# Kernel optimization log

Measured on AMD Instinct MI355X. Metric: run time of the kernel, lower is better.

The kernel has to match this reference:

```python
import jax, jax.numpy as jnp
import numpy as np

B, N, DIM = 4, 8192, 512
HEADS, DIM_HEAD = 8, 64
INNER = HEADS * DIM_HEAD
SCALE = DIM_HEAD ** -0.5


def setup_inputs() -> dict:
    key = jax.random.key(0)
    ks = jax.random.split(key, 8)
    return {
        "x": jax.random.normal(ks[0], (B, N, DIM), jnp.float32),
        "mask": jnp.zeros((B, N), jnp.bool_),
        "W_qkv": jax.random.normal(ks[1], (3 * INNER, DIM), jnp.float32) * 0.02,
        "w_q_logits": jax.random.normal(ks[2], (DIM_HEAD,), jnp.float32) * 0.02,
        "w_k_logits": jax.random.normal(ks[3], (DIM_HEAD,), jnp.float32) * 0.02,
        "W_r": jax.random.normal(ks[4], (DIM_HEAD, DIM_HEAD), jnp.float32) * 0.02,
        "b_r": jnp.zeros((DIM_HEAD,), jnp.float32),
        "W_out": jax.random.normal(ks[5], (DIM, INNER), jnp.float32) * 0.02,
        "b_out": jnp.zeros((DIM,), jnp.float32),
    }


def reference(x, mask, W_qkv, w_q_logits, w_k_logits, W_r, b_r, W_out, b_out):
    b, n, _ = x.shape
    neg_inf = jnp.float32(-jnp.inf)
    qkv = x @ W_qkv.T                              # (b, n, 3*inner)
    q, k, v = jnp.split(qkv, 3, axis=-1)           # each (b, n, inner)
    # faithful to torch: contiguous().view(b, heads, n, dim_head) == plain reshape
    q = q.reshape(b, HEADS, n, DIM_HEAD)
    k = k.reshape(b, HEADS, n, DIM_HEAD)
    v = v.reshape(b, HEADS, n, DIM_HEAD)
    m = mask[:, None, :]                           # (b, 1, n)

    # query pooling -> global query vector
    q_logits = jnp.einsum('bhnd,d->bhn', q, w_q_logits) * SCALE
    q_attn = jax.nn.softmax(jnp.where(m, neg_inf, q_logits), axis=-1)
    global_q = jnp.einsum('bhn,bhnd->bhd', q_attn, q)   # (b, h, d)

    # gate keys with global query, pool -> global key vector
    kg = k * global_q[:, :, None, :]
    k_logits = jnp.einsum('bhnd,d->bhn', kg, w_k_logits) * SCALE
    k_attn = jax.nn.softmax(jnp.where(m, neg_inf, k_logits), axis=-1)
    global_k = jnp.einsum('bhn,bhnd->bhd', k_attn, k)   # pools original k (k_agg)

    # gate values with global key, project, residual with q
    vg = v * global_k[:, :, None, :]
    r = vg @ W_r.T + b_r + q                            # (b, h, n, d)
    r = r.reshape(b, n, INNER)
    return r @ W_out.T + b_out
```

## Files before the change

kernel.cpp:

```cpp
#include <hip/hip_runtime.h>
#include <cstdint>

#define NB    4
#define NSEQ  8192
#define NDIM  512
#define NHEAD 8
#define DH    64
#define NTOK  (NB * NSEQ)
#define QKV_W 1536
#define SCALE 0.125f

typedef unsigned short u16;
typedef __attribute__((ext_vector_type(8))) unsigned short u16x8;
typedef __attribute__((ext_vector_type(4))) unsigned short u16x4;
typedef __attribute__((ext_vector_type(8))) short s16x8;
typedef __attribute__((ext_vector_type(4))) float f32x4;

__device__ __forceinline__ float bf2f(u16 u) {
  return __uint_as_float(((unsigned int)u) << 16);
}
__device__ __forceinline__ u16 f2bf(float f) {
  unsigned int x = __float_as_uint(f);
  x += 0x7fffu + ((x >> 16) & 1u);
  return (u16)(x >> 16);
}
__device__ __forceinline__ void gload_lds16(const void* g, void* l) {
  __builtin_amdgcn_global_load_lds(
      (const __attribute__((address_space(1))) unsigned int*)g,
      (__attribute__((address_space(3))) unsigned int*)l, 16, 0, 0);
}

__global__ __launch_bounds__(256) void cvt_bf16(
    const float* __restrict__ s0, u16* __restrict__ d0, int n0,
    const float* __restrict__ s1, u16* __restrict__ d1, int n1,
    const float* __restrict__ s2, u16* __restrict__ d2, int n2) {
  int gid = blockIdx.x * 256 + threadIdx.x;
  int stride = gridDim.x * 256;
  int t0 = n0 >> 2, t1 = n1 >> 2, t2 = n2 >> 2;
  for (int i = gid; i < t0; i += stride) {
    f32x4 v = ((const f32x4*)s0)[i];
    u16x4 o; o[0]=f2bf(v[0]); o[1]=f2bf(v[1]); o[2]=f2bf(v[2]); o[3]=f2bf(v[3]);
    ((u16x4*)d0)[i] = o;
  }
  for (int i = gid; i < t1; i += stride) {
    f32x4 v = ((const f32x4*)s1)[i];
    u16x4 o; o[0]=f2bf(v[0]); o[1]=f2bf(v[1]); o[2]=f2bf(v[2]); o[3]=f2bf(v[3]);
    ((u16x4*)d1)[i] = o;
  }
  for (int i = gid; i < t2; i += stride) {
    f32x4 v = ((const f32x4*)s2)[i];
    u16x4 o; o[0]=f2bf(v[0]); o[1]=f2bf(v[1]); o[2]=f2bf(v[2]); o[3]=f2bf(v[3]);
    ((u16x4*)d2)[i] = o;
  }
}

__global__ __launch_bounds__(512, 2) void gemm256(
    const u16* __restrict__ A, const u16* __restrict__ B,
    int K, int tiles_n,
    u16* __restrict__ Cbf, float* __restrict__ Cf,
    const float* __restrict__ bias) {
  __shared__ u16 lds[65536];
  const int KT = K >> 6;

  const int nwg = gridDim.x, bid = blockIdx.x;
  const int cpx = nwg >> 3;
  const int swz = (bid & 7) * cpx + (bid >> 3);
  const int tm = swz / tiles_n, tn = swz - tm * tiles_n;

  const int tid = threadIdx.x, lane = tid & 63, wid = tid >> 6;
  const int wm = wid >> 2, wn = wid & 3;
  const int rA = lane & 15, kq = lane >> 4, swl = lane & 7;

  const u16* Ab = A + (size_t)tm * 256 * K;
  const u16* Bb = B + (size_t)tn * 256 * K;

  auto STAGE = [&](int isB, int d, int h, int kt) {
    const u16* src = isB ? Bb : Ab;
    const int base = (isB ? 32768 : 0) + (d * 2 + h) * 8192;
#pragma unroll
    for (int r = 0; r < 2; ++r) {
      const int slot = r * 512 + tid;
      const int row = slot >> 3, ch = slot & 7;
      gload_lds16(src + (size_t)(h * 128 + row) * K + kt * 64 +
                      ((ch ^ (row & 7)) << 3),
                  &lds[base + slot * 8]);
    }
  };

  f32x4 acc[8][4] = {};

  STAGE(0, 0, 0, 0); STAGE(0, 0, 1, 0);
  STAGE(1, 0, 0, 0); STAGE(1, 0, 1, 0);
  {
    const int k1 = (KT > 1) ? 1 : 0;
    STAGE(1, 1, 0, k1); STAGE(1, 1, 1, k1);
  }
  asm volatile("s_waitcnt vmcnt(4)" ::: "memory");
  __builtin_amdgcn_s_barrier();

#define LDA(m, kk) (*(const s16x8*)&lds[Abase + ((m) * 16 + rA) * 64 + \
                                        ((((kk) * 4 + kq) ^ swl) << 3)])
#define LDB(n, kk) (*(const s16x8*)&lds[Bbase + (brow + (n) * 16 + rA) * 64 + \
                                        ((((kk) * 4 + kq) ^ swl) << 3)])
#define MFMA_(a, b, c) __builtin_amdgcn_mfma_f32_16x16x32_bf16(a, b, c, 0, 0, 0)

#define PHASE(M0, M1, BREAD, STG, TAIL)                                  \
  {                                                                      \
    s16x8 a00 = LDA(M0, 0), a01 = LDA(M0, 1);                            \
    s16x8 a10 = LDA(M1, 0), a11 = LDA(M1, 1);                            \
    BREAD                                                                \
    STG                                                                  \
    __builtin_amdgcn_s_barrier();                                        \
    asm volatile("s_waitcnt lgkmcnt(0)" ::: "memory");                   \
    __builtin_amdgcn_s_setprio(1);                                       \
    acc[M0][0] = MFMA_(a00, b00, acc[M0][0]);                            \
    acc[M0][0] = MFMA_(a01, b01, acc[M0][0]);                            \
    acc[M0][1] = MFMA_(a00, b10, acc[M0][1]);                            \
    acc[M0][1] = MFMA_(a01, b11, acc[M0][1]);                            \
    acc[M0][2] = MFMA_(a00, b20, acc[M0][2]);                            \
    acc[M0][2] = MFMA_(a01, b21, acc[M0][2]);                            \
    acc[M0][3] = MFMA_(a00, b30, acc[M0][3]);                            \
    acc[M0][3] = MFMA_(a01, b31, acc[M0][3]);                            \
    acc[M1][0] = MFMA_(a10, b00, acc[M1][0]);                            \
    acc[M1][0] = MFMA_(a11, b01, acc[M1][0]);                            \
    acc[M1][1] = MFMA_(a10, b10, acc[M1][1]);                            \
    acc[M1][1] = MFMA_(a11, b11, acc[M1][1]);                            \
    acc[M1][2] = MFMA_(a10, b20, acc[M1][2]);                            \
    acc[M1][2] = MFMA_(a11, b21, acc[M1][2]);                            \
    acc[M1][3] = MFMA_(a10, b30, acc[M1][3]);                            \
    acc[M1][3] = MFMA_(a11, b31, acc[M1][3]);                            \
    __builtin_amdgcn_s_setprio(0);                                       \
    TAIL                                                                 \
    __builtin_amdgcn_s_barrier();                                        \
  }

  for (int t = 0; t < KT; ++t) {
    const int d = t & 1;
    const int kA = (t + 1 < KT) ? t + 1 : KT - 1;
    const int kB = (t + 2 < KT) ? t + 2 : KT - 1;
    const int Abase = (d * 2 + wm) * 8192;
    const int Bbase = 32768 + (d * 2 + (wn >> 1)) * 8192;
    const int brow = (wn & 1) * 64;

    s16x8 b00, b01, b10, b11, b20, b21, b30, b31;

    PHASE(0, 1,
          { b00 = LDB(0, 0); b01 = LDB(0, 1); b10 = LDB(1, 0); b11 = LDB(1, 1);
            b20 = LDB(2, 0); b21 = LDB(2, 1); b30 = LDB(3, 0); b31 = LDB(3, 1); },
          STAGE(0, d ^ 1, 0, kA);, )
    PHASE(2, 3, , STAGE(0, d ^ 1, 1, kA);, )
    PHASE(4, 5, , STAGE(1, d, 0, kB);, )
    PHASE(6, 7, , STAGE(1, d, 1, kB);,
          asm volatile("s_waitcnt vmcnt(4)" ::: "memory");)
  }

  asm volatile("s_waitcnt vmcnt(0)" ::: "memory");

  const int crow = kq * 4;
  const int ccol = rA;
  const size_t row_base = (size_t)tm * 256 + wm * 128;
  const int col_base = tn * 256 + wn * 64;
  const int N = tiles_n << 8;
  if (Cbf) {
#pragma unroll
    for (int m = 0; m < 8; ++m)
#pragma unroll
      for (int n = 0; n < 4; ++n)
#pragma unroll
        for (int j = 0; j < 4; ++j)
          Cbf[(row_base + m * 16 + crow + j) * N + col_base + n * 16 + ccol] =
              f2bf(acc[m][n][j]);
  } else {
#pragma unroll
    for (int m = 0; m < 8; ++m)
#pragma unroll
      for (int n = 0; n < 4; ++n) {
        int col = col_base + n * 16 + ccol;
        float bv = bias[col];
#pragma unroll
        for (int j = 0; j < 4; ++j)
          Cf[(row_base + m * 16 + crow + j) * N + col] = acc[m][n][j] + bv;
      }
  }
#undef LDA
#undef LDB
#undef MFMA_
#undef PHASE
}

__global__ __launch_bounds__(256) void pool_stage(
    const u16* __restrict__ qkv, int chan_off,
    const float* __restrict__ wvec, float scale,
    float* __restrict__ partS, float* __restrict__ partG) {
  __shared__ float redG[4][64];
  __shared__ float redS[4];
  const int bid = blockIdx.x;
  const int bh = bid >> 3, chunk = bid & 7;
  const int b = bh >> 3, h = bh & 7;
  const int tid = threadIdx.x, lane = tid & 63, w = tid >> 6;
  const int j = lane & 7;

  float wreg[8];
#pragma unroll
  for (int i = 0; i < 8; ++i) wreg[i] = wvec[j * 8 + i];

  float accS = 0.f;
  float accG[8] = {};
  const size_t tok0 = (size_t)b * NSEQ + (size_t)h * 1024 + chunk * 128;

  for (int it = 0; it < 32; ++it) {
    const u16* row = qkv + (tok0 + it * 4 + w) * QKV_W + chan_off;
    u16x8 q8 = *(const u16x8*)(row + lane * 8);
    float qf[8];
#pragma unroll
    for (int i = 0; i < 8; ++i) qf[i] = bf2f(q8[i]);
    float dot = 0.f;
#pragma unroll
    for (int i = 0; i < 8; ++i) dot += qf[i] * wreg[i];
    dot += __shfl_xor(dot, 1);
    dot += __shfl_xor(dot, 2);
    dot += __shfl_xor(dot, 4);
    float e = __expf(dot * scale);
    accS += (j == 0) ? e : 0.f;
#pragma unroll
    for (int i = 0; i < 8; ++i) accG[i] += e * qf[i];
  }
#pragma unroll
  for (int m = 8; m <= 32; m <<= 1) {
    accS += __shfl_xor(accS, m);
#pragma unroll
    for (int i = 0; i < 8; ++i) accG[i] += __shfl_xor(accG[i], m);
  }
  if (lane < 8) {
#pragma unroll
    for (int i = 0; i < 8; ++i) redG[w][lane * 8 + i] = accG[i];
    if (lane == 0) redS[w] = accS;
  }
  __syncthreads();
  if (tid < 64) {
    float G = redG[0][tid] + redG[1][tid] + redG[2][tid] + redG[3][tid];
    partG[(size_t)bid * 64 + tid] = G;
    if (tid == 0) partS[bid] = redS[0] + redS[1] + redS[2] + redS[3];
  }
}

__global__ __launch_bounds__(64) void finalize_pool(
    const float* __restrict__ partS, const float* __restrict__ partG,
    const float* __restrict__ mulvec, float scale,
    float* __restrict__ outv) {
  int bh = blockIdx.x, d = threadIdx.x;
  float S = 0.f, G = 0.f;
#pragma unroll
  for (int c = 0; c < 8; ++c) {
    S += partS[bh * 8 + c];
    G += partG[(bh * 8 + c) * 64 + d];
  }
  float g = G / S;
  if (mulvec) g *= mulvec[d] * scale;
  outv[bh * 64 + d] = g;
}

__global__ __launch_bounds__(256) void r_stage(
    const u16* __restrict__ qkv, const float* __restrict__ gk,
    const float* __restrict__ W_r, const float* __restrict__ b_r,
    u16* __restrict__ rout) {
  __shared__ float M2T[64 * 64];
  const int t0 = blockIdx.x * 32;
  const int bh = (t0 >> 13) * 8 + ((t0 & 8191) >> 10);
  const int tid = threadIdx.x;
  for (int idx = tid; idx < 4096; idx += 256) {
    int e = idx >> 6, d = idx & 63;
    M2T[idx] = W_r[d * 64 + e] * gk[bh * 64 + e];
  }
  __syncthreads();

  const int t = t0 + (tid >> 3), g = tid & 7;
  const u16* vrow = qkv + (size_t)t * QKV_W + 1024 + g * 64;
  const u16* qrow = qkv + (size_t)t * QKV_W + g * 64;

  f32x4 acc[16] = {};
  for (int ec = 0; ec < 8; ++ec) {
    u16x8 v8 = *(const u16x8*)(vrow + ec * 8);
#pragma unroll
    for (int eo = 0; eo < 8; ++eo) {
      float ve = bf2f(v8[eo]);
      const f32x4* m2row = (const f32x4*)(M2T + (ec * 8 + eo) * 64);
#pragma unroll
      for (int c4 = 0; c4 < 16; ++c4) acc[c4] += ve * m2row[c4];
    }
  }
#pragma unroll
  for (int i = 0; i < 8; ++i) {
    u16x8 q8 = *(const u16x8*)(qrow + i * 8);
    u16x8 o;
#pragma unroll
    for (int ii = 0; ii < 8; ++ii) {
      int d = i * 8 + ii;
      float val = bf2f(q8[ii]) + b_r[d] + acc[d >> 2][d & 3];
      o[ii] = f2bf(val);
    }
    *(u16x8*)(rout + (size_t)t * NDIM + g * 64 + i * 8) = o;
  }
}

extern "C" void kernel_launch(void* const* d_in, const int* in_sizes, int n_in,
                              void* d_out, int out_size, void* d_ws,
                              size_t ws_size, hipStream_t stream) {
  const float* x    = (const float*)d_in[0];
  const float* Wqkv = (const float*)d_in[2];
  const float* wq   = (const float*)d_in[3];
  const float* wk   = (const float*)d_in[4];
  const float* Wr   = (const float*)d_in[5];
  const float* br   = (const float*)d_in[6];
  const float* Wout = (const float*)d_in[7];
  const float* bout = (const float*)d_in[8];
  float* out = (float*)d_out;

  char* w = (char*)d_ws;
  auto carve = [&](size_t bytes) {
    char* p = w;
    w += (bytes + 255) & ~(size_t)255;
    return p;
  };
  u16* x_bf    = (u16*)carve((size_t)NTOK * NDIM * 2);
  u16* qkv_bf  = (u16*)carve((size_t)NTOK * QKV_W * 2);
  u16* Wqkv_bf = (u16*)carve((size_t)QKV_W * NDIM * 2);
  u16* Wout_bf = (u16*)carve((size_t)NDIM * NDIM * 2);
  float* partS  = (float*)carve(256 * 4);
  float* partG  = (float*)carve(256 * 64 * 4);
  float* wk_eff = (float*)carve(32 * 64 * 4);
  float* gk     = (float*)carve(32 * 64 * 4);
  u16* r_bf    = x_bf;

  cvt_bf16<<<2048, 256, 0, stream>>>(x, x_bf, NTOK * NDIM,
                                     Wqkv, Wqkv_bf, QKV_W * NDIM,
                                     Wout, Wout_bf, NDIM * NDIM);
  gemm256<<<128 * 6, 512, 0, stream>>>(x_bf, Wqkv_bf, NDIM, 6,
                                       qkv_bf, nullptr, nullptr);
  pool_stage<<<256, 256, 0, stream>>>(qkv_bf, 0, wq, SCALE, partS, partG);
  finalize_pool<<<32, 64, 0, stream>>>(partS, partG, wk, SCALE, wk_eff);
  pool_stage<<<256, 256, 0, stream>>>(qkv_bf, 512, wk_eff, 1.0f, partS, partG);
  finalize_pool<<<32, 64, 0, stream>>>(partS, partG, nullptr, 1.0f, gk);
  r_stage<<<NTOK / 32, 256, 0, stream>>>(qkv_bf, gk, Wr, br, r_bf);
  gemm256<<<128 * 2, 512, 0, stream>>>(r_bf, Wout_bf, NDIM, 2,
                                       nullptr, out, bout);
}
```

Measured before the change: 318.5 us.

## Compute gated value projection with bf16 MFMA instead of scalar FMA

The r-stage scalar fp32 FMA loop over a shared-memory M2T matrix is replaced by a small prep kernel and an MFMA kernel. The prep kernel folds the global-key gate into W_r per (batch, head) and stores it as bf16. The MFMA kernel keeps those weights in registers and runs 16x16x32 bf16 MFMAs over rows of V. This moves the per-token 64x64 matmul off the vector ALUs and removes the LDS staging, at the cost of one extra launch and rounding the gated weights to bf16.

```diff
diff --git a/kernel.cpp b/kernel.cpp
--- a/kernel.cpp
+++ b/kernel.cpp
@@ -260,47 +260,72 @@
   outv[bh * 64 + d] = g;
 }
 
-__global__ __launch_bounds__(256) void r_stage(
-    const u16* __restrict__ qkv, const float* __restrict__ gk,
-    const float* __restrict__ W_r, const float* __restrict__ b_r,
-    u16* __restrict__ rout) {
-  __shared__ float M2T[64 * 64];
-  const int t0 = blockIdx.x * 32;
-  const int bh = (t0 >> 13) * 8 + ((t0 & 8191) >> 10);
-  const int tid = threadIdx.x;
-  for (int idx = tid; idx < 4096; idx += 256) {
-    int e = idx >> 6, d = idx & 63;
-    M2T[idx] = W_r[d * 64 + e] * gk[bh * 64 + e];
-  }
-  __syncthreads();
-
-  const int t = t0 + (tid >> 3), g = tid & 7;
-  const u16* vrow = qkv + (size_t)t * QKV_W + 1024 + g * 64;
-  const u16* qrow = qkv + (size_t)t * QKV_W + g * 64;
-
-  f32x4 acc[16] = {};
-  for (int ec = 0; ec < 8; ++ec) {
-    u16x8 v8 = *(const u16x8*)(vrow + ec * 8);
-#pragma unroll
-    for (int eo = 0; eo < 8; ++eo) {
-      float ve = bf2f(v8[eo]);
-      const f32x4* m2row = (const f32x4*)(M2T + (ec * 8 + eo) * 64);
-#pragma unroll
-      for (int c4 = 0; c4 < 16; ++c4) acc[c4] += ve * m2row[c4];
+__global__ __launch_bounds__(256) void weff_prep(
+    const float* __restrict__ Wr, const float* __restrict__ gk,
+    u16* __restrict__ weff) {
+  const int bh = blockIdx.x, tid = threadIdx.x;
+  for (int i = tid; i < 4096; i += 256) {
+    int e = i & 63;
+    weff[bh * 4096 + i] = f2bf(Wr[i] * gk[bh * 64 + e]);
+  }
+}
+
+__global__ __launch_bounds__(256) void r_mfma(
+    const u16* __restrict__ qkv, const u16* __restrict__ weff,
+    const float* __restrict__ b_r, u16* __restrict__ rout) {
+  const int tid = threadIdx.x, lane = tid & 63, wv = tid >> 6;
+  const size_t rho0 = (size_t)blockIdx.x * 256 + wv * 64;
+  const int bh = (int)(rho0 >> 13);
+  const int rA = lane & 15, kq = lane >> 4;
+
+#define MFMA_(a, b, c) __builtin_amdgcn_mfma_f32_16x16x32_bf16(a, b, c, 0, 0, 0)
+
+  s16x8 af[4][2];
+  const u16* wb = weff + bh * 4096;
+#pragma unroll
+  for (int fm = 0; fm < 4; ++fm)
+#pragma unroll
+    for (int kk = 0; kk < 2; ++kk)
+      af[fm][kk] = *(const s16x8*)(wb + (fm * 16 + rA) * 64 + kk * 32 + kq * 8);
+
+  f32x4 br4[4];
+#pragma unroll
+  for (int fm = 0; fm < 4; ++fm)
+    br4[fm] = *(const f32x4*)(b_r + fm * 16 + kq * 4);
+
+  f32x4 acc[4][4] = {};
+#pragma unroll
+  for (int fn = 0; fn < 4; ++fn) {
+    const size_t rho = rho0 + fn * 16 + rA;
+    const u16* vr = qkv + (rho >> 3) * QKV_W + 1024 + (rho & 7) * 64;
+    s16x8 b0 = *(const s16x8*)(vr + kq * 8);
+    s16x8 b1 = *(const s16x8*)(vr + 32 + kq * 8);
+#pragma unroll
+    for (int fm = 0; fm < 4; ++fm) {
+      acc[fm][fn] = MFMA_(af[fm][0], b0, acc[fm][fn]);
+      acc[fm][fn] = MFMA_(af[fm][1], b1, acc[fm][fn]);
     }
   }
-#pragma unroll
-  for (int i = 0; i < 8; ++i) {
-    u16x8 q8 = *(const u16x8*)(qrow + i * 8);
-    u16x8 o;
-#pragma unroll
-    for (int ii = 0; ii < 8; ++ii) {
-      int d = i * 8 + ii;
-      float val = bf2f(q8[ii]) + b_r[d] + acc[d >> 2][d & 3];
-      o[ii] = f2bf(val);
+
+#pragma unroll
+  for (int fn = 0; fn < 4; ++fn) {
+    const size_t rho = rho0 + fn * 16 + rA;
+    const size_t t = rho >> 3;
+    const int g = (int)(rho & 7);
+    const u16* qr = qkv + t * QKV_W + g * 64;
+    u16* orow = rout + t * NDIM + g * 64;
+#pragma unroll
+    for (int fm = 0; fm < 4; ++fm) {
+      const int d0 = fm * 16 + kq * 4;
+      u16x4 q4 = *(const u16x4*)(qr + d0);
+      u16x4 o;
+#pragma unroll
+      for (int j = 0; j < 4; ++j)
+        o[j] = f2bf(acc[fm][fn][j] + br4[fm][j] + bf2f(q4[j]));
+      *(u16x4*)(orow + d0) = o;
     }
-    *(u16x8*)(rout + (size_t)t * NDIM + g * 64 + i * 8) = o;
-  }
+  }
+#undef MFMA_
 }
 
 extern "C" void kernel_launch(void* const* d_in, const int* in_sizes, int n_in,
@@ -330,6 +355,7 @@
   float* partG  = (float*)carve(256 * 64 * 4);
   float* wk_eff = (float*)carve(32 * 64 * 4);
   float* gk     = (float*)carve(32 * 64 * 4);
+  u16* weff    = (u16*)carve(32 * 64 * 64 * 2);
   u16* r_bf    = x_bf;
 
   cvt_bf16<<<2048, 256, 0, stream>>>(x, x_bf, NTOK * NDIM,
@@ -341,7 +367,8 @@
   finalize_pool<<<32, 64, 0, stream>>>(partS, partG, wk, SCALE, wk_eff);
   pool_stage<<<256, 256, 0, stream>>>(qkv_bf, 512, wk_eff, 1.0f, partS, partG);
   finalize_pool<<<32, 64, 0, stream>>>(partS, partG, nullptr, 1.0f, gk);
-  r_stage<<<NTOK / 32, 256, 0, stream>>>(qkv_bf, gk, Wr, br, r_bf);
+  weff_prep<<<32, 256, 0, stream>>>(Wr, gk, weff);
+  r_mfma<<<NTOK * 8 / 256, 256, 0, stream>>>(qkv_bf, weff, br, r_bf);
   gemm256<<<128 * 2, 512, 0, stream>>>(r_bf, Wout_bf, NDIM, 2,
                                        nullptr, out, bout);
 }
```

Result: faster. 274.7 us (-13.8%).

## Fold W_r and global-key gating into per-head output weights, drop r_stage

Applied to the files above, without the earlier changes.

Precomputes P = W_out·blockdiag(W_r) and a combined bias vector, then builds per-(batch,head-group) concatenated weights that fold the global-key gating into P. The final GEMM reads v and q directly from the qkv buffer with K=1024, which removes the r_stage kernel and its intermediate write and read. The pooling stages are also split into 4x more blocks for parallelism. The cost is doubling K in the output GEMM, 32 per-batch weight copies, and an extra prep computation over the weight matrices.

```diff
diff --git a/kernel.cpp b/kernel.cpp
--- a/kernel.cpp
+++ b/kernel.cpp
@@ -30,27 +30,41 @@
       (__attribute__((address_space(3))) unsigned int*)l, 16, 0, 0);
 }
 
-__global__ __launch_bounds__(256) void cvt_bf16(
-    const float* __restrict__ s0, u16* __restrict__ d0, int n0,
-    const float* __restrict__ s1, u16* __restrict__ d1, int n1,
-    const float* __restrict__ s2, u16* __restrict__ d2, int n2) {
+__global__ __launch_bounds__(256) void prep(
+    const float* __restrict__ x, u16* __restrict__ x_bf,
+    const float* __restrict__ Wqkv, u16* __restrict__ Wqkv_bf,
+    const float* __restrict__ Wout, const float* __restrict__ Wr,
+    float* __restrict__ P,
+    const float* __restrict__ br, const float* __restrict__ bout,
+    float* __restrict__ cvec) {
   int gid = blockIdx.x * 256 + threadIdx.x;
   int stride = gridDim.x * 256;
-  int t0 = n0 >> 2, t1 = n1 >> 2, t2 = n2 >> 2;
+  int t0 = (NTOK * NDIM) >> 2;
   for (int i = gid; i < t0; i += stride) {
-    f32x4 v = ((const f32x4*)s0)[i];
+    f32x4 v = ((const f32x4*)x)[i];
     u16x4 o; o[0]=f2bf(v[0]); o[1]=f2bf(v[1]); o[2]=f2bf(v[2]); o[3]=f2bf(v[3]);
-    ((u16x4*)d0)[i] = o;
-  }
+    ((u16x4*)x_bf)[i] = o;
+  }
+  int t1 = (QKV_W * NDIM) >> 2;
   for (int i = gid; i < t1; i += stride) {
-    f32x4 v = ((const f32x4*)s1)[i];
+    f32x4 v = ((const f32x4*)Wqkv)[i];
     u16x4 o; o[0]=f2bf(v[0]); o[1]=f2bf(v[1]); o[2]=f2bf(v[2]); o[3]=f2bf(v[3]);
-    ((u16x4*)d1)[i] = o;
-  }
-  for (int i = gid; i < t2; i += stride) {
-    f32x4 v = ((const f32x4*)s2)[i];
-    u16x4 o; o[0]=f2bf(v[0]); o[1]=f2bf(v[1]); o[2]=f2bf(v[2]); o[3]=f2bf(v[3]);
-    ((u16x4*)d2)[i] = o;
+    ((u16x4*)Wqkv_bf)[i] = o;
+  }
+  for (int i = gid; i < 512 * 512; i += stride) {
+    int o = i >> 9, ii = i & 511;
+    int g = ii >> 6, e = ii & 63;
+    const float* wo = Wout + o * 512 + g * 64;
+    float s = 0.f;
+#pragma unroll 8
+    for (int d = 0; d < 64; ++d) s += wo[d] * Wr[d * 64 + e];
+    P[i] = s;
+  }
+  for (int o = gid; o < 512; o += stride) {
+    float s = bout[o];
+    const float* wo = Wout + o * 512;
+    for (int i2 = 0; i2 < 512; ++i2) s += wo[i2] * br[i2 & 63];
+    cvec[o] = s;
   }
 }
 
@@ -188,6 +202,133 @@
 #undef PHASE
 }
 
+__global__ __launch_bounds__(512, 2) void gemm_out(
+    const u16* __restrict__ qkv, const u16* __restrict__ Wcat,
+    const float* __restrict__ cvec, float* __restrict__ out) {
+  __shared__ u16 lds[65536];
+  const int KT = 16;
+
+  const int nwg = gridDim.x, bid = blockIdx.x;
+  const int cpx = nwg >> 3;
+  const int swz = (bid & 7) * cpx + (bid >> 3);
+  const int tm = swz >> 1, tn = swz & 1;
+
+  const int tid = threadIdx.x, lane = tid & 63, wid = tid >> 6;
+  const int wm = wid >> 2, wn = wid & 3;
+  const int rA = lane & 15, kq = lane >> 4, swl = lane & 7;
+
+  const u16* Bb = Wcat + ((size_t)(tm >> 2) * 512 + tn * 256) * 1024;
+
+  auto STAGEA = [&](int d, int h, int kt) {
+    const int base = (d * 2 + h) * 8192;
+    const int col0 = (kt < 8) ? (1024 + kt * 64) : ((kt - 8) * 64);
+#pragma unroll
+    for (int r = 0; r < 2; ++r) {
+      const int slot = r * 512 + tid;
+      const int row = slot >> 3, ch = slot & 7;
+      gload_lds16(qkv + (size_t)(tm * 256 + h * 128 + row) * QKV_W + col0 +
+                      ((ch ^ (row & 7)) << 3),
+                  &lds[base + slot * 8]);
+    }
+  };
+  auto STAGEB = [&](int d, int h, int kt) {
+    const int base = 32768 + (d * 2 + h) * 8192;
+#pragma unroll
+    for (int r = 0; r < 2; ++r) {
+      const int slot = r * 512 + tid;
+      const int row = slot >> 3, ch = slot & 7;
+      gload_lds16(Bb + (size_t)(h * 128 + row) * 1024 + kt * 64 +
+                      ((ch ^ (row & 7)) << 3),
+                  &lds[base + slot * 8]);
+    }
+  };
+
+  f32x4 acc[8][4] = {};
+
+  STAGEA(0, 0, 0); STAGEA(0, 1, 0);
+  STAGEB(0, 0, 0); STAGEB(0, 1, 0);
+  STAGEB(1, 0, 1); STAGEB(1, 1, 1);
+  asm volatile("s_waitcnt vmcnt(4)" ::: "memory");
+  __builtin_amdgcn_s_barrier();
+
+#define LDA(m, kk) (*(const s16x8*)&lds[Abase + ((m) * 16 + rA) * 64 + \
+                                        ((((kk) * 4 + kq) ^ swl) << 3)])
+#define LDB(n, kk) (*(const s16x8*)&lds[Bbase + (brow + (n) * 16 + rA) * 64 + \
+                                        ((((kk) * 4 + kq) ^ swl) << 3)])
+#define MFMA_(a, b, c) __builtin_amdgcn_mfma_f32_16x16x32_bf16(a, b, c, 0, 0, 0)
+
+#define PHASE(M0, M1, BREAD, STG, TAIL)                                  \
+  {                                                                      \
+    s16x8 a00 = LDA(M0, 0), a01 = LDA(M0, 1);                            \
+    s16x8 a10 = LDA(M1, 0), a11 = LDA(M1, 1);                            \
+    BREAD                                                                \
+    STG                                                                  \
+    __builtin_amdgcn_s_barrier();                                        \
+    asm volatile("s_waitcnt lgkmcnt(0)" ::: "memory");                   \
+    __builtin_amdgcn_s_setprio(1);                                       \
+    acc[M0][0] = MFMA_(a00, b00, acc[M0][0]);                            \
+    acc[M0][0] = MFMA_(a01, b01, acc[M0][0]);                            \
+    acc[M0][1] = MFMA_(a00, b10, acc[M0][1]);                            \
+    acc[M0][1] = MFMA_(a01, b11, acc[M0][1]);                            \
+    acc[M0][2] = MFMA_(a00, b20, acc[M0][2]);                            \
+    acc[M0][2] = MFMA_(a01, b21, acc[M0][2]);                            \
+    acc[M0][3] = MFMA_(a00, b30, acc[M0][3]);                            \
+    acc[M0][3] = MFMA_(a01, b31, acc[M0][3]);                            \
+    acc[M1][0] = MFMA_(a10, b00, acc[M1][0]);                            \
+    acc[M1][0] = MFMA_(a11, b01, acc[M1][0]);                            \
+    acc[M1][1] = MFMA_(a10, b10, acc[M1][1]);                            \
+    acc[M1][1] = MFMA_(a11, b11, acc[M1][1]);                            \
+    acc[M1][2] = MFMA_(a10, b20, acc[M1][2]);                            \
+    acc[M1][2] = MFMA_(a11, b21, acc[M1][2]);                            \
+    acc[M1][3] = MFMA_(a10, b30, acc[M1][3]);                            \
+    acc[M1][3] = MFMA_(a11, b31, acc[M1][3]);                            \
+    __builtin_amdgcn_s_setprio(0);                                       \
+    TAIL                                                                 \
+    __builtin_amdgcn_s_barrier();                                        \
+  }
+
+  for (int t = 0; t < KT; ++t) {
+    const int d = t & 1;
+    const int kA = (t + 1 < KT) ? t + 1 : KT - 1;
+    const int kB = (t + 2 < KT) ? t + 2 : KT - 1;
+    const int Abase = (d * 2 + wm) * 8192;
+    const int Bbase = 32768 + (d * 2 + (wn >> 1)) * 8192;
+    const int brow = (wn & 1) * 64;
+
+    s16x8 b00, b01, b10, b11, b20, b21, b30, b31;
+
+    PHASE(0, 1,
+          { b00 = LDB(0, 0); b01 = LDB(0, 1); b10 = LDB(1, 0); b11 = LDB(1, 1);
+            b20 = LDB(2, 0); b21 = LDB(2, 1); b30 = LDB(3, 0); b31 = LDB(3, 1); },
+          STAGEA(d ^ 1, 0, kA);, )
+    PHASE(2, 3, , STAGEA(d ^ 1, 1, kA);, )
+    PHASE(4, 5, , STAGEB(d, 0, kB);, )
+    PHASE(6, 7, , STAGEB(d, 1, kB);,
+          asm volatile("s_waitcnt vmcnt(4)" ::: "memory");)
+  }
+
+  asm volatile("s_waitcnt vmcnt(0)" ::: "memory");
+
+  const int crow = kq * 4;
+  const int ccol = rA;
+  const size_t row_base = (size_t)tm * 256 + wm * 128;
+  const int col_base = tn * 256 + wn * 64;
+#pragma unroll
+  for (int m = 0; m < 8; ++m)
+#pragma unroll
+    for (int n = 0; n < 4; ++n) {
+      int col = col_base + n * 16 + ccol;
+      float bv = cvec[col];
+#pragma unroll
+      for (int j = 0; j < 4; ++j)
+        out[(row_base + m * 16 + crow + j) * NDIM + col] = acc[m][n][j] + bv;
+    }
+#undef LDA
+#undef LDB
+#undef MFMA_
+#undef PHASE
+}
+
 __global__ __launch_bounds__(256) void pool_stage(
     const u16* __restrict__ qkv, int chan_off,
     const float* __restrict__ wvec, float scale,
@@ -195,7 +336,7 @@
   __shared__ float redG[4][64];
   __shared__ float redS[4];
   const int bid = blockIdx.x;
-  const int bh = bid >> 3, chunk = bid & 7;
+  const int bh = bid >> 5, chunk = bid & 31;
   const int b = bh >> 3, h = bh & 7;
   const int tid = threadIdx.x, lane = tid & 63, w = tid >> 6;
   const int j = lane & 7;
@@ -206,9 +347,9 @@
 
   float accS = 0.f;
   float accG[8] = {};
-  const size_t tok0 = (size_t)b * NSEQ + (size_t)h * 1024 + chunk * 128;
-
-  for (int it = 0; it < 32; ++it) {
+  const size_t tok0 = (size_t)b * NSEQ + (size_t)h * 1024 + chunk * 32;
+
+  for (int it = 0; it < 8; ++it) {
     const u16* row = qkv + (tok0 + it * 4 + w) * QKV_W + chan_off;
     u16x8 q8 = *(const u16x8*)(row + lane * 8);
     float qf[8];
@@ -251,55 +392,47 @@
   int bh = blockIdx.x, d = threadIdx.x;
   float S = 0.f, G = 0.f;
 #pragma unroll
-  for (int c = 0; c < 8; ++c) {
-    S += partS[bh * 8 + c];
-    G += partG[(bh * 8 + c) * 64 + d];
+  for (int c = 0; c < 32; ++c) {
+    S += partS[bh * 32 + c];
+    G += partG[(size_t)(bh * 32 + c) * 64 + d];
   }
   float g = G / S;
   if (mulvec) g *= mulvec[d] * scale;
   outv[bh * 64 + d] = g;
 }
 
-__global__ __launch_bounds__(256) void r_stage(
-    const u16* __restrict__ qkv, const float* __restrict__ gk,
-    const float* __restrict__ W_r, const float* __restrict__ b_r,
-    u16* __restrict__ rout) {
-  __shared__ float M2T[64 * 64];
-  const int t0 = blockIdx.x * 32;
-  const int bh = (t0 >> 13) * 8 + ((t0 & 8191) >> 10);
-  const int tid = threadIdx.x;
-  for (int idx = tid; idx < 4096; idx += 256) {
-    int e = idx >> 6, d = idx & 63;
-    M2T[idx] = W_r[d * 64 + e] * gk[bh * 64 + e];
+__global__ __launch_bounds__(256) void wcat_prep(
+    const float* __restrict__ partS, const float* __restrict__ partG,
+    const float* __restrict__ P, const float* __restrict__ Wout,
+    u16* __restrict__ Wcat) {
+  __shared__ float gkd[64];
+  const int blk = blockIdx.x, tid = threadIdx.x;
+  const int bh = blk >> 3, ng = blk & 7;
+  if (tid < 64) {
+    float s = 0.f, g = 0.f;
+#pragma unroll
+    for (int c = 0; c < 32; ++c) {
+      s += partS[bh * 32 + c];
+      g += partG[(size_t)(bh * 32 + c) * 64 + tid];
+    }
+    gkd[tid] = g / s;
   }
   __syncthreads();
-
-  const int t = t0 + (tid >> 3), g = tid & 7;
-  const u16* vrow = qkv + (size_t)t * QKV_W + 1024 + g * 64;
-  const u16* qrow = qkv + (size_t)t * QKV_W + g * 64;
-
-  f32x4 acc[16] = {};
-  for (int ec = 0; ec < 8; ++ec) {
-    u16x8 v8 = *(const u16x8*)(vrow + ec * 8);
-#pragma unroll
-    for (int eo = 0; eo < 8; ++eo) {
-      float ve = bf2f(v8[eo]);
-      const f32x4* m2row = (const f32x4*)(M2T + (ec * 8 + eo) * 64);
-#pragma unroll
-      for (int c4 = 0; c4 < 16; ++c4) acc[c4] += ve * m2row[c4];
-    }
-  }
-#pragma unroll
-  for (int i = 0; i < 8; ++i) {
-    u16x8 q8 = *(const u16x8*)(qrow + i * 8);
-    u16x8 o;
-#pragma unroll
-    for (int ii = 0; ii < 8; ++ii) {
-      int d = i * 8 + ii;
-      float val = bf2f(q8[ii]) + b_r[d] + acc[d >> 2][d & 3];
-      o[ii] = f2bf(val);
-    }
-    *(u16x8*)(rout + (size_t)t * NDIM + g * 64 + i * 8) = o;
+  const int n0 = ng * 64;
+  for (int i = tid; i < 64 * 256; i += 256) {
+    int r = i >> 8, k0 = (i & 255) * 4;
+    int n = n0 + r;
+    u16x4 o;
+    if (k0 < 512) {
+      const float* pr = P + n * 512 + k0;
+#pragma unroll
+      for (int j = 0; j < 4; ++j) o[j] = f2bf(pr[j] * gkd[(k0 + j) & 63]);
+    } else {
+      const float* wr = Wout + n * 512 + (k0 - 512);
+#pragma unroll
+      for (int j = 0; j < 4; ++j) o[j] = f2bf(wr[j]);
+    }
+    *(u16x4*)(Wcat + ((size_t)bh * 512 + n) * 1024 + k0) = o;
   }
 }
 
@@ -325,23 +458,20 @@
   u16* x_bf    = (u16*)carve((size_t)NTOK * NDIM * 2);
   u16* qkv_bf  = (u16*)carve((size_t)NTOK * QKV_W * 2);
   u16* Wqkv_bf = (u16*)carve((size_t)QKV_W * NDIM * 2);
-  u16* Wout_bf = (u16*)carve((size_t)NDIM * NDIM * 2);
-  float* partS  = (float*)carve(256 * 4);
-  float* partG  = (float*)carve(256 * 64 * 4);
+  float* partS  = (float*)carve(1024 * 4);
+  float* partG  = (float*)carve(1024 * 64 * 4);
   float* wk_eff = (float*)carve(32 * 64 * 4);
-  float* gk     = (float*)carve(32 * 64 * 4);
-  u16* r_bf    = x_bf;
-
-  cvt_bf16<<<2048, 256, 0, stream>>>(x, x_bf, NTOK * NDIM,
-                                     Wqkv, Wqkv_bf, QKV_W * NDIM,
-                                     Wout, Wout_bf, NDIM * NDIM);
+  float* P      = (float*)carve(512 * 512 * 4);
+  float* cvec   = (float*)carve(512 * 4);
+  u16* Wcat    = (u16*)carve((size_t)32 * 512 * 1024 * 2);
+
+  prep<<<2048, 256, 0, stream>>>(x, x_bf, Wqkv, Wqkv_bf,
+                                 Wout, Wr, P, br, bout, cvec);
   gemm256<<<128 * 6, 512, 0, stream>>>(x_bf, Wqkv_bf, NDIM, 6,
                                        qkv_bf, nullptr, nullptr);
-  pool_stage<<<256, 256, 0, stream>>>(qkv_bf, 0, wq, SCALE, partS, partG);
+  pool_stage<<<1024, 256, 0, stream>>>(qkv_bf, 0, wq, SCALE, partS, partG);
   finalize_pool<<<32, 64, 0, stream>>>(partS, partG, wk, SCALE, wk_eff);
-  pool_stage<<<256, 256, 0, stream>>>(qkv_bf, 512, wk_eff, 1.0f, partS, partG);
-  finalize_pool<<<32, 64, 0, stream>>>(partS, partG, nullptr, 1.0f, gk);
-  r_stage<<<NTOK / 32, 256, 0, stream>>>(qkv_bf, gk, Wr, br, r_bf);
-  gemm256<<<128 * 2, 512, 0, stream>>>(r_bf, Wout_bf, NDIM, 2,
-                                       nullptr, out, bout);
-}
+  pool_stage<<<1024, 256, 0, stream>>>(qkv_bf, 512, wk_eff, 1.0f, partS, partG);
+  wcat_prep<<<256, 256, 0, stream>>>(partS, partG, P, Wout, Wcat);
+  gemm_out<<<256, 512, 0, stream>>>(qkv_bf, Wcat, cvec, out);
+}
```

Result: faster. 300.2 us (-5.8%).
